# Kernel tuning notes

Hardware: AMD Instinct MI355X
Metric: run time of the kernel (lower is better)

Reference implementation:

```python
import jax, jax.numpy as jnp
import numpy as np

N, C, K, STEPS = 131072, 256, 5, 20


def setup_inputs() -> dict:
    key = jax.random.key(0)
    k1, k2, k3, k4 = jax.random.split(key, 4)
    drive = jax.random.uniform(k1, (N, C), dtype=jnp.float32)  # sigmoid-like drive in [0,1]
    K_raw = jax.random.uniform(k2, (K,), dtype=jnp.float32)
    K_local = K_raw / K_raw.sum()  # positive, sums to 1
    W = jax.random.uniform(k3, (C, C), dtype=jnp.float32)
    mask = (jax.random.uniform(k4, (C, C)) < 0.2).astype(jnp.float32)
    W = W * mask
    W_cc = W / jnp.clip(W.sum(axis=0, keepdims=True), 1e-8)  # column-stochastic
    r = jnp.full((C,), 3.9, dtype=jnp.float32)
    eps = jnp.full((C,), 0.3, dtype=jnp.float32)
    beta = jnp.full((C,), 0.1, dtype=jnp.float32)
    return {"drive": drive, "r": r, "eps": eps, "beta": beta,
            "K_local": K_local, "W_cc": W_cc}


def reference(drive, r, eps, beta, K_local, W_cc):
    # readout == 'final' (module default)
    pad = K // 2
    one_m_eps = 1.0 - eps
    one_m_beta = 1.0 - beta

    def step(grid, _):
        mapped = r * grid * (1.0 - grid)  # [N, C] logistic map
        # circular conv1d over channel axis (cross-correlation, kernel K_local)
        local = K_local[0] * jnp.roll(mapped, pad, axis=-1)
        for j in range(1, K):
            local = local + K_local[j] * jnp.roll(mapped, pad - j, axis=-1)
        global_cc = mapped @ W_cc  # [N, C]
        coupled = 0.5 * (local + global_cc)
        physics = one_m_eps * mapped + eps * coupled
        new_grid = one_m_beta * physics + beta * drive
        return new_grid, None

    grid, _ = jax.lax.scan(step, drive, None, length=STEPS)
    return jnp.clip(grid, 1e-4, 1.0 - 1e-4)
```

## Files before the change

kernel.cpp:

```cpp
#include <hip/hip_runtime.h>

#define C_DIM 256
#define STEPS 20
#define ROWS_PER_WG 32
#define LDS_ROW 640
#define PLANE 20480
#define BUFSZ 40960
#define SMEM_TOT 81920

typedef _Float16 f16;
typedef f16 f16x4 __attribute__((ext_vector_type(4)));
typedef f16 f16x8 __attribute__((ext_vector_type(8)));
typedef float f32x4 __attribute__((ext_vector_type(4)));

__global__ __launch_bounds__(256) void prep_w(const float* __restrict__ W,
                                              const float* __restrict__ Kl,
                                              const float* __restrict__ eps_,
                                              const float* __restrict__ beta_,
                                              f16* __restrict__ whi,
                                              f16* __restrict__ wlo)
{
    const int f = (int)(blockIdx.x * blockDim.x + threadIdx.x) >> 6;
    const int l = (int)threadIdx.x & 63;
    if (f >= 128) return;
    const float P2 = (1.0f - beta_[0]) * eps_[0];
    const int mt = f >> 3, kb = f & 7;
    const int n = mt * 16 + (l & 15);
    const int kbase = kb * 32 + (l >> 4) * 8;
    f16 h[8], lo[8];
    #pragma unroll
    for (int j = 0; j < 8; ++j) {
        const int k = kbase + j;
        float v = 0.5f * W[k * C_DIM + n];
        const int d = (k - n + 2) & (C_DIM - 1);
        if (d < 5) v += 0.5f * Kl[d];
        v *= P2;
        const f16 hh = (f16)v;
        h[j] = hh;
        lo[j] = (f16)((v - (float)hh) * 4096.0f);
    }
    const size_t off = (size_t)f * 512 + (size_t)l * 8;
    *(f16x8*)(whi + off) = *(f16x8*)h;
    *(f16x8*)(wlo + off) = *(f16x8*)lo;
}

__global__ __launch_bounds__(512, 2) void cml_main(
    const float* __restrict__ drive,
    const float* __restrict__ r_,
    const float* __restrict__ eps_,
    const float* __restrict__ beta_,
    const f16* __restrict__ whi,
    const f16* __restrict__ wlo,
    float* __restrict__ out)
{
    extern __shared__ char smem[];

    const int tid = (int)threadIdx.x;
    const int w   = tid >> 6;
    const int l   = tid & 63;
    const int kg  = l >> 4;
    const int cl  = l & 15;
    const size_t rowBase = (size_t)blockIdx.x * ROWS_PER_WG;

    f16x8 Wh[2][8], Wl[2][8];
    #pragma unroll
    for (int mti = 0; mti < 2; ++mti) {
        #pragma unroll
        for (int kb = 0; kb < 8; ++kb) {
            const size_t off = (size_t)((w * 2 + mti) * 8 + kb) * 512 + (size_t)l * 8;
            Wh[mti][kb] = *(const f16x8*)(whi + off);
            Wl[mti][kb] = *(const f16x8*)(wlo + off);
        }
    }

    const float r0 = r_[0];
    const float e0 = eps_[0];
    const float b0 = beta_[0];
    const float P1s = (1.0f - b0) * (1.0f - e0);

    float gm[2][2][4], drv[2][2][4];
    #pragma unroll
    for (int mti = 0; mti < 2; ++mti) {
        const int ch0 = (w * 2 + mti) * 16 + kg * 4;
        #pragma unroll
        for (int nt = 0; nt < 2; ++nt) {
            const size_t row = rowBase + (size_t)(nt * 16 + cl);
            const f32x4 d4 = *(const f32x4*)(drive + row * C_DIM + ch0);
            #pragma unroll
            for (int r = 0; r < 4; ++r) {
                gm[mti][nt][r]  = d4[r];
                drv[mti][nt][r] = b0 * d4[r];
            }
        }
    }

    int rdb[2], woff[2][2];
    #pragma unroll
    for (int nt = 0; nt < 2; ++nt) {
        const int m = nt * 16 + cl;
        rdb[nt] = m * LDS_ROW + ((kg + (m & 7)) << 4);
        #pragma unroll
        for (int mti = 0; mti < 2; ++mti) {
            const int c = (w * 2 + mti) * 2 + (kg >> 1);
            woff[mti][nt] = m * LDS_ROW + ((c + (m & 7)) << 4) + ((kg & 1) << 3);
        }
    }

    #pragma unroll
    for (int mti = 0; mti < 2; ++mti) {
        #pragma unroll
        for (int nt = 0; nt < 2; ++nt) {
            float mv[4];
            #pragma unroll
            for (int r = 0; r < 4; ++r) {
                const float gv = gm[mti][nt][r];
                mv[r] = r0 * gv * (1.0f - gv);
                gm[mti][nt][r] = mv[r];
            }
            const auto h01 = __builtin_amdgcn_cvt_pkrtz(mv[0], mv[1]);
            const auto h23 = __builtin_amdgcn_cvt_pkrtz(mv[2], mv[3]);
            const auto l01 = __builtin_amdgcn_cvt_pkrtz(
                (mv[0] - (float)h01[0]) * 4096.0f, (mv[1] - (float)h01[1]) * 4096.0f);
            const auto l23 = __builtin_amdgcn_cvt_pkrtz(
                (mv[2] - (float)h23[0]) * 4096.0f, (mv[3] - (float)h23[1]) * 4096.0f);
            f16x4 hv, lv;
            hv[0] = (f16)h01[0]; hv[1] = (f16)h01[1]; hv[2] = (f16)h23[0]; hv[3] = (f16)h23[1];
            lv[0] = (f16)l01[0]; lv[1] = (f16)l01[1]; lv[2] = (f16)l23[0]; lv[3] = (f16)l23[1];
            *(f16x4*)(smem + woff[mti][nt]) = hv;
            *(f16x4*)(smem + woff[mti][nt] + PLANE) = lv;
        }
    }

    #pragma unroll 1
    for (int s = 0; s < STEPS; ++s) {
        __syncthreads();
        const int rb = (s & 1) * BUFSZ;
        const int wbuf = BUFSZ - rb;
        const int lastStep = (s == STEPS - 1);

        #pragma unroll
        for (int nt = 0; nt < 2; ++nt) {
            f32x4 acch[2], accl[2], accm[2];
            #pragma unroll
            for (int mti = 0; mti < 2; ++mti) {
                #pragma unroll
                for (int r = 0; r < 4; ++r) {
                    acch[mti][r] = fmaf(P1s, gm[mti][nt][r], drv[mti][nt][r]);
                    accl[mti][r] = 0.0f;
                    accm[mti][r] = 0.0f;
                }
            }

            const char* rp = smem + rb + rdb[nt];
            #pragma unroll
            for (int kb = 0; kb < 8; ++kb) {
                const f16x8 bh = *(const f16x8*)(rp + kb * 64);
                const f16x8 bl = *(const f16x8*)(rp + kb * 64 + PLANE);
                #pragma unroll
                for (int mti = 0; mti < 2; ++mti) {
                    acch[mti] = __builtin_amdgcn_mfma_f32_16x16x32_f16(Wh[mti][kb], bh, acch[mti], 0, 0, 0);
                    accl[mti] = __builtin_amdgcn_mfma_f32_16x16x32_f16(Wl[mti][kb], bh, accl[mti], 0, 0, 0);
                    accm[mti] = __builtin_amdgcn_mfma_f32_16x16x32_f16(Wh[mti][kb], bl, accm[mti], 0, 0, 0);
                }
            }

            #pragma unroll
            for (int mti = 0; mti < 2; ++mti) {
                float mv[4];
                #pragma unroll
                for (int r = 0; r < 4; ++r) {
                    const float gn = fmaf(accl[mti][r] + accm[mti][r],
                                          1.0f / 4096.0f, acch[mti][r]);
                    if (lastStep) {
                        gm[mti][nt][r] = gn;
                    } else {
                        mv[r] = r0 * gn * (1.0f - gn);
                        gm[mti][nt][r] = mv[r];
                    }
                }
                if (!lastStep) {
                    const auto h01 = __builtin_amdgcn_cvt_pkrtz(mv[0], mv[1]);
                    const auto h23 = __builtin_amdgcn_cvt_pkrtz(mv[2], mv[3]);
                    const auto l01 = __builtin_amdgcn_cvt_pkrtz(
                        (mv[0] - (float)h01[0]) * 4096.0f, (mv[1] - (float)h01[1]) * 4096.0f);
                    const auto l23 = __builtin_amdgcn_cvt_pkrtz(
                        (mv[2] - (float)h23[0]) * 4096.0f, (mv[3] - (float)h23[1]) * 4096.0f);
                    f16x4 hv, lv;
                    hv[0] = (f16)h01[0]; hv[1] = (f16)h01[1]; hv[2] = (f16)h23[0]; hv[3] = (f16)h23[1];
                    lv[0] = (f16)l01[0]; lv[1] = (f16)l01[1]; lv[2] = (f16)l23[0]; lv[3] = (f16)l23[1];
                    *(f16x4*)(smem + wbuf + woff[mti][nt]) = hv;
                    *(f16x4*)(smem + wbuf + woff[mti][nt] + PLANE) = lv;
                }
            }
        }
    }

    #pragma unroll
    for (int mti = 0; mti < 2; ++mti) {
        const int ch0 = (w * 2 + mti) * 16 + kg * 4;
        #pragma unroll
        for (int nt = 0; nt < 2; ++nt) {
            const size_t row = rowBase + (size_t)(nt * 16 + cl);
            f32x4 o;
            #pragma unroll
            for (int r = 0; r < 4; ++r) {
                o[r] = fminf(fmaxf(gm[mti][nt][r], 1e-4f), 1.0f - 1e-4f);
            }
            *(f32x4*)(out + row * C_DIM + ch0) = o;
        }
    }
}

extern "C" void kernel_launch(void* const* d_in, const int* in_sizes, int n_in,
                              void* d_out, int out_size, void* d_ws, size_t ws_size,
                              hipStream_t stream) {
    (void)n_in; (void)ws_size; (void)out_size;
    const float* drive = (const float*)d_in[0];
    const float* r     = (const float*)d_in[1];
    const float* eps   = (const float*)d_in[2];
    const float* beta  = (const float*)d_in[3];
    const float* Kl    = (const float*)d_in[4];
    const float* W     = (const float*)d_in[5];
    float* out = (float*)d_out;

    f16* whi = (f16*)d_ws;
    f16* wlo = whi + 65536;

    prep_w<<<dim3(32), dim3(256), 0, stream>>>(W, Kl, eps, beta, whi, wlo);

    (void)hipFuncSetAttribute((const void*)cml_main,
                        hipFuncAttributeMaxDynamicSharedMemorySize, SMEM_TOT);

    const int nrows = in_sizes[0] / C_DIM;
    cml_main<<<dim3((unsigned)(nrows / ROWS_PER_WG)), dim3(512), SMEM_TOT, stream>>>(
        drive, r, eps, beta, whi, wlo, out);
}
```

Before: 715.7 us.

## Interleave epilogue of first row tile with MFMAs of second, spill drive to LDS

The per-step loop is hand-unrolled so the elementwise tail (logistic map, hi/lo fp16 split, LDS writes) for the first row tile is interleaved between the MFMA groups of the second row tile. This hides VALU and LDS-store latency behind matrix work. The per-thread drive term is moved from registers into a new LDS region and reloaded during the tail, and the next-step accumulator init is precomputed there. The goal is to cut register pressure and serial epilogue time, at the cost of extra LDS traffic and a larger shared-memory footprint that may limit the two-blocks-per-CU occupancy.

```diff
diff --git a/kernel.cpp b/kernel.cpp
--- a/kernel.cpp
+++ b/kernel.cpp
@@ -6,12 +6,15 @@
 #define LDS_ROW 640
 #define PLANE 20480
 #define BUFSZ 40960
-#define SMEM_TOT 81920
+#define DRV_OFF 81920
+#define SMEM_TOT (81920 + 512 * 80)
 
 typedef _Float16 f16;
 typedef f16 f16x4 __attribute__((ext_vector_type(4)));
 typedef f16 f16x8 __attribute__((ext_vector_type(8)));
 typedef float f32x4 __attribute__((ext_vector_type(4)));
+
+#define MFMA16 __builtin_amdgcn_mfma_f32_16x16x32_f16
 
 __global__ __launch_bounds__(256) void prep_w(const float* __restrict__ W,
                                               const float* __restrict__ Kl,
@@ -61,6 +64,7 @@
     const int kg  = l >> 4;
     const int cl  = l & 15;
     const size_t rowBase = (size_t)blockIdx.x * ROWS_PER_WG;
+    const int drvBase = DRV_OFF + tid * 80;
 
     f16x8 Wh[2][8], Wl[2][8];
     #pragma unroll
@@ -78,7 +82,20 @@
     const float b0 = beta_[0];
     const float P1s = (1.0f - b0) * (1.0f - e0);
 
-    float gm[2][2][4], drv[2][2][4];
+    int rdb[2], woff[2][2];
+    #pragma unroll
+    for (int nt = 0; nt < 2; ++nt) {
+        const int m = nt * 16 + cl;
+        rdb[nt] = m * LDS_ROW + ((kg + (m & 7)) << 4);
+        #pragma unroll
+        for (int mti = 0; mti < 2; ++mti) {
+            const int c = (w * 2 + mti) * 2 + (kg >> 1);
+            woff[mti][nt] = m * LDS_ROW + ((c + (m & 7)) << 4) + ((kg & 1) << 3);
+        }
+    }
+
+    float gm[2][2][4];
+    f32x4 A0[2], A1[2];
     #pragma unroll
     for (int mti = 0; mti < 2; ++mti) {
         const int ch0 = (w * 2 + mti) * 16 + kg * 4;
@@ -86,37 +103,16 @@
         for (int nt = 0; nt < 2; ++nt) {
             const size_t row = rowBase + (size_t)(nt * 16 + cl);
             const f32x4 d4 = *(const f32x4*)(drive + row * C_DIM + ch0);
-            #pragma unroll
-            for (int r = 0; r < 4; ++r) {
-                gm[mti][nt][r]  = d4[r];
-                drv[mti][nt][r] = b0 * d4[r];
-            }
-        }
-    }
-
-    int rdb[2], woff[2][2];
-    #pragma unroll
-    for (int nt = 0; nt < 2; ++nt) {
-        const int m = nt * 16 + cl;
-        rdb[nt] = m * LDS_ROW + ((kg + (m & 7)) << 4);
-        #pragma unroll
-        for (int mti = 0; mti < 2; ++mti) {
-            const int c = (w * 2 + mti) * 2 + (kg >> 1);
-            woff[mti][nt] = m * LDS_ROW + ((c + (m & 7)) << 4) + ((kg & 1) << 3);
-        }
-    }
-
-    #pragma unroll
-    for (int mti = 0; mti < 2; ++mti) {
-        #pragma unroll
-        for (int nt = 0; nt < 2; ++nt) {
+            f32x4 dv;
             float mv[4];
             #pragma unroll
             for (int r = 0; r < 4; ++r) {
-                const float gv = gm[mti][nt][r];
+                dv[r] = b0 * d4[r];
+                const float gv = d4[r];
                 mv[r] = r0 * gv * (1.0f - gv);
                 gm[mti][nt][r] = mv[r];
             }
+            *(f32x4*)(smem + drvBase + ((mti * 2 + nt) << 4)) = dv;
             const auto h01 = __builtin_amdgcn_cvt_pkrtz(mv[0], mv[1]);
             const auto h23 = __builtin_amdgcn_cvt_pkrtz(mv[2], mv[3]);
             const auto l01 = __builtin_amdgcn_cvt_pkrtz(
@@ -128,71 +124,89 @@
             lv[0] = (f16)l01[0]; lv[1] = (f16)l01[1]; lv[2] = (f16)l23[0]; lv[3] = (f16)l23[1];
             *(f16x4*)(smem + woff[mti][nt]) = hv;
             *(f16x4*)(smem + woff[mti][nt] + PLANE) = lv;
-        }
-    }
+            f32x4 ai;
+            #pragma unroll
+            for (int r = 0; r < 4; ++r) ai[r] = fmaf(P1s, mv[r], dv[r]);
+            if (nt == 0) A0[mti] = ai; else A1[mti] = ai;
+        }
+    }
+
+#define GSTEP(RP, AA, LL, MM, KB) do {                                        \
+    const f16x8 bh_ = *(const f16x8*)((RP) + (KB) * 64);                      \
+    const f16x8 bl_ = *(const f16x8*)((RP) + (KB) * 64 + PLANE);              \
+    AA[0] = MFMA16(Wh[0][KB], bh_, AA[0], 0, 0, 0);                           \
+    AA[1] = MFMA16(Wh[1][KB], bh_, AA[1], 0, 0, 0);                           \
+    LL[0] = MFMA16(Wl[0][KB], bh_, LL[0], 0, 0, 0);                           \
+    LL[1] = MFMA16(Wl[1][KB], bh_, LL[1], 0, 0, 0);                           \
+    MM[0] = MFMA16(Wh[0][KB], bl_, MM[0], 0, 0, 0);                           \
+    MM[1] = MFMA16(Wh[1][KB], bl_, MM[1], 0, 0, 0);                           \
+} while (0)
+
+#define TAIL(NT, MTI, AV, LACC, MACC) do {                                    \
+    float mv[4];                                                              \
+    _Pragma("unroll")                                                         \
+    for (int r = 0; r < 4; ++r) {                                             \
+        const float gn = fmaf(LACC[r] + MACC[r], 1.0f / 4096.0f, AV[r]);      \
+        if (lastStep) { gm[MTI][NT][r] = gn; }                                \
+        else { mv[r] = r0 * gn * (1.0f - gn); gm[MTI][NT][r] = mv[r]; }       \
+    }                                                                         \
+    if (!lastStep) {                                                          \
+        const auto h01 = __builtin_amdgcn_cvt_pkrtz(mv[0], mv[1]);            \
+        const auto h23 = __builtin_amdgcn_cvt_pkrtz(mv[2], mv[3]);            \
+        const auto l01 = __builtin_amdgcn_cvt_pkrtz(                          \
+            (mv[0] - (float)h01[0]) * 4096.0f, (mv[1] - (float)h01[1]) * 4096.0f); \
+        const auto l23 = __builtin_amdgcn_cvt_pkrtz(                          \
+            (mv[2] - (float)h23[0]) * 4096.0f, (mv[3] - (float)h23[1]) * 4096.0f); \
+        f16x4 hv, lv;                                                         \
+        hv[0] = (f16)h01[0]; hv[1] = (f16)h01[1];                             \
+        hv[2] = (f16)h23[0]; hv[3] = (f16)h23[1];                             \
+        lv[0] = (f16)l01[0]; lv[1] = (f16)l01[1];                             \
+        lv[2] = (f16)l23[0]; lv[3] = (f16)l23[1];                             \
+        *(f16x4*)(smem + wbuf + woff[MTI][NT]) = hv;                          \
+        *(f16x4*)(smem + wbuf + woff[MTI][NT] + PLANE) = lv;                  \
+        const f32x4 dv = *(const f32x4*)(smem + drvBase + ((MTI * 2 + NT) << 4)); \
+        _Pragma("unroll")                                                     \
+        for (int r = 0; r < 4; ++r) AV[r] = fmaf(P1s, mv[r], dv[r]);          \
+    }                                                                         \
+} while (0)
 
     #pragma unroll 1
     for (int s = 0; s < STEPS; ++s) {
         __syncthreads();
         const int rb = (s & 1) * BUFSZ;
         const int wbuf = BUFSZ - rb;
-        const int lastStep = (s == STEPS - 1);
-
-        #pragma unroll
-        for (int nt = 0; nt < 2; ++nt) {
-            f32x4 acch[2], accl[2], accm[2];
-            #pragma unroll
-            for (int mti = 0; mti < 2; ++mti) {
-                #pragma unroll
-                for (int r = 0; r < 4; ++r) {
-                    acch[mti][r] = fmaf(P1s, gm[mti][nt][r], drv[mti][nt][r]);
-                    accl[mti][r] = 0.0f;
-                    accm[mti][r] = 0.0f;
-                }
-            }
-
-            const char* rp = smem + rb + rdb[nt];
-            #pragma unroll
-            for (int kb = 0; kb < 8; ++kb) {
-                const f16x8 bh = *(const f16x8*)(rp + kb * 64);
-                const f16x8 bl = *(const f16x8*)(rp + kb * 64 + PLANE);
-                #pragma unroll
-                for (int mti = 0; mti < 2; ++mti) {
-                    acch[mti] = __builtin_amdgcn_mfma_f32_16x16x32_f16(Wh[mti][kb], bh, acch[mti], 0, 0, 0);
-                    accl[mti] = __builtin_amdgcn_mfma_f32_16x16x32_f16(Wl[mti][kb], bh, accl[mti], 0, 0, 0);
-                    accm[mti] = __builtin_amdgcn_mfma_f32_16x16x32_f16(Wh[mti][kb], bl, accm[mti], 0, 0, 0);
-                }
-            }
-
-            #pragma unroll
-            for (int mti = 0; mti < 2; ++mti) {
-                float mv[4];
-                #pragma unroll
-                for (int r = 0; r < 4; ++r) {
-                    const float gn = fmaf(accl[mti][r] + accm[mti][r],
-                                          1.0f / 4096.0f, acch[mti][r]);
-                    if (lastStep) {
-                        gm[mti][nt][r] = gn;
-                    } else {
-                        mv[r] = r0 * gn * (1.0f - gn);
-                        gm[mti][nt][r] = mv[r];
-                    }
-                }
-                if (!lastStep) {
-                    const auto h01 = __builtin_amdgcn_cvt_pkrtz(mv[0], mv[1]);
-                    const auto h23 = __builtin_amdgcn_cvt_pkrtz(mv[2], mv[3]);
-                    const auto l01 = __builtin_amdgcn_cvt_pkrtz(
-                        (mv[0] - (float)h01[0]) * 4096.0f, (mv[1] - (float)h01[1]) * 4096.0f);
-                    const auto l23 = __builtin_amdgcn_cvt_pkrtz(
-                        (mv[2] - (float)h23[0]) * 4096.0f, (mv[3] - (float)h23[1]) * 4096.0f);
-                    f16x4 hv, lv;
-                    hv[0] = (f16)h01[0]; hv[1] = (f16)h01[1]; hv[2] = (f16)h23[0]; hv[3] = (f16)h23[1];
-                    lv[0] = (f16)l01[0]; lv[1] = (f16)l01[1]; lv[2] = (f16)l23[0]; lv[3] = (f16)l23[1];
-                    *(f16x4*)(smem + wbuf + woff[mti][nt]) = hv;
-                    *(f16x4*)(smem + wbuf + woff[mti][nt] + PLANE) = lv;
-                }
-            }
-        }
+        const bool lastStep = (s == STEPS - 1);
+        const char* rp0 = smem + rb + rdb[0];
+        const char* rp1 = smem + rb + rdb[1];
+
+        f32x4 L0[2], M0[2];
+        L0[0] = (f32x4)0.0f; L0[1] = (f32x4)0.0f;
+        M0[0] = (f32x4)0.0f; M0[1] = (f32x4)0.0f;
+        GSTEP(rp0, A0, L0, M0, 0);
+        GSTEP(rp0, A0, L0, M0, 1);
+        GSTEP(rp0, A0, L0, M0, 2);
+        GSTEP(rp0, A0, L0, M0, 3);
+        GSTEP(rp0, A0, L0, M0, 4);
+        GSTEP(rp0, A0, L0, M0, 5);
+        GSTEP(rp0, A0, L0, M0, 6);
+        GSTEP(rp0, A0, L0, M0, 7);
+
+        f32x4 L1[2], M1[2];
+        L1[0] = (f32x4)0.0f; L1[1] = (f32x4)0.0f;
+        M1[0] = (f32x4)0.0f; M1[1] = (f32x4)0.0f;
+        GSTEP(rp1, A1, L1, M1, 0);
+        GSTEP(rp1, A1, L1, M1, 1);
+        GSTEP(rp1, A1, L1, M1, 2);
+        TAIL(0, 0, A0[0], L0[0], M0[0]);
+        GSTEP(rp1, A1, L1, M1, 3);
+        GSTEP(rp1, A1, L1, M1, 4);
+        GSTEP(rp1, A1, L1, M1, 5);
+        TAIL(0, 1, A0[1], L0[1], M0[1]);
+        GSTEP(rp1, A1, L1, M1, 6);
+        GSTEP(rp1, A1, L1, M1, 7);
+
+        TAIL(1, 0, A1[0], L1[0], M1[0]);
+        TAIL(1, 1, A1[1], L1[1], M1[1]);
     }
 
     #pragma unroll
```

After: 1.048 ms. 46.4% more time.
